# Optimization experiments

Hardware: AMD Instinct MI355X
Metric: run time of the kernel (lower is better)

Reference implementation:

```python
import jax, jax.numpy as jnp
import numpy as np

K = 5  # kernel_size per dim
# 2^dim = 4 active degree-1 B-spline products per edge (dim=2)
BITS = jnp.array([[0, 0], [1, 0], [0, 1], [1, 1]], dtype=jnp.int32)  # [S,2]


def spline_basis(edge_attr):
    """Open B-spline basis, degree=1, dim=2, kernel_size=5 per dim.
    Returns basis weights [E,S] and flattened kernel indices [E,S]."""
    v = edge_attr * (K - 1)                 # scale pseudo-coords to knot grid
    i0 = jnp.floor(v)
    f = v - i0                              # fractional part, [E,2]
    # per-dim linear weights: f for bit=1, (1-f) for bit=0
    w = jnp.where(BITS[None] == 1, f[:, None, :], 1.0 - f[:, None, :])  # [E,S,2]
    basis = w[..., 0] * w[..., 1]           # [E,S]
    idx = jnp.minimum(i0.astype(jnp.int32)[:, None, :] + BITS[None], K - 1)  # [E,S,2]
    kidx = idx[..., 0] + K * idx[..., 1]    # flatten 2D kernel index -> [0,25)
    return basis, kidx


def spline_conv(x, src, dst, basis, kidx, W, root, bias, n):
    # transform-then-gather: y[n,k,:] = x[n] @ W[k]
    y = jnp.einsum('ni,kio->nko', x, W)                 # [N,25,out]
    g = y[src[:, None], kidx]                           # gather [E,S,out]
    msg = jnp.einsum('es,eso->eo', basis, g)            # weighted sum over S
    agg = jax.ops.segment_sum(msg, dst, num_segments=n)  # scatter-add to targets
    return agg + x @ root + bias                        # root weight + bias


def setup_inputs() -> dict:
    key = jax.random.key(0)
    ks = jax.random.split(key, 8)
    N, E, IN, H, OUT = 50000, 400000, 32, 64, 64
    x = jax.random.normal(ks[0], (N, IN), jnp.float32)
    edge_index = jax.random.randint(ks[1], (2, E), 0, N, dtype=jnp.int32)
    edge_attr = jax.random.uniform(ks[2], (E, 2), jnp.float32)

    def glorot(k, shape):
        fan = shape[-2] + shape[-1]
        return jax.random.normal(k, shape, jnp.float32) * jnp.sqrt(2.0 / fan)

    W1 = glorot(ks[3], (K * K, IN, H));  root1 = glorot(ks[4], (IN, H));  b1 = jnp.zeros((H,), jnp.float32)
    W2 = glorot(ks[5], (K * K, H, OUT)); root2 = glorot(ks[6], (H, OUT)); b2 = jnp.zeros((OUT,), jnp.float32)
    fc_w = glorot(ks[7], (OUT, 3));      fc_b = jnp.zeros((3,), jnp.float32)
    return dict(x=x, edge_index=edge_index, edge_attr=edge_attr,
                W1=W1, root1=root1, b1=b1, W2=W2, root2=root2, b2=b2,
                fc_w=fc_w, fc_b=fc_b)


def reference(x, edge_index, edge_attr, W1, root1, b1, W2, root2, b2, fc_w, fc_b):
    # eval-mode forward (dropout is identity at inference)
    n = x.shape[0]
    src, dst = edge_index[0], edge_index[1]
    basis, kidx = spline_basis(edge_attr)
    h = jax.nn.relu(spline_conv(x, src, dst, basis, kidx, W1, root1, b1, n))
    h = jax.nn.relu(spline_conv(h, src, dst, basis, kidx, W2, root2, b2, n))
    return h @ fc_w + fc_b
```

## Files before the change

kernel.cpp:

```cpp
#include <hip/hip_runtime.h>
#include <stdint.h>

typedef __attribute__((ext_vector_type(8))) short short8;
typedef __attribute__((ext_vector_type(4))) float f32x4;
typedef __attribute__((ext_vector_type(4))) unsigned short ushort4v;

#define CHUNK 512

__device__ __forceinline__ unsigned short f2bf(float f) {
    unsigned int u = __float_as_uint(f);
    u = (u + 0x7FFFu + ((u >> 16) & 1u)) >> 16;
    return (unsigned short)u;
}
__device__ __forceinline__ float bf2f(unsigned short h) {
    return __uint_as_float(((unsigned int)h) << 16);
}
__device__ __forceinline__ int cell_of(float ax, float ay) {
    int c0 = (int)floorf(ax * 4.f); c0 = min(max(c0, 0), 3);
    int c1 = (int)floorf(ay * 4.f); c1 = min(max(c1, 0), 3);
    return c0 + 4 * c1;
}

__global__ __launch_bounds__(256) void zero_kernel(int* __restrict__ p, int n) {
    int t = blockIdx.x * 256 + threadIdx.x;
    if (t < n) p[t] = 0;
}

template<int KIN>
__device__ __forceinline__ void pack_cell_elem(const float* __restrict__ W,
                                               unsigned short* __restrict__ pkc, int u) {
    constexpr int KCH = KIN / 8;
    if (u >= 16 * 4 * KCH * 512) return;
    int low9 = u & 511;
    int grp  = u >> 9;
    int kc = grp % KCH; grp /= KCH;
    int c  = grp & 3;
    int cell = grp >> 2;
    int lane = low9 >> 3, j = low9 & 7;
    int k = kc * 32 + (lane >> 4) * 8 + j;
    int t = k / KIN, i = k % KIN;
    int k0 = (cell & 3) + (t & 1);   if (k0 > 4) k0 = 4;
    int k1 = (cell >> 2) + (t >> 1); if (k1 > 4) k1 = 4;
    float val = W[((size_t)(k0 + 5 * k1) * KIN + i) * 64 + (c * 16 + (lane & 15))];
    pkc[u] = f2bf(val);
}

template<int KIN>
__device__ __forceinline__ void pack_root_elem(const float* __restrict__ root,
                                               unsigned short* __restrict__ pkr, int u) {
    constexpr int KCHr = KIN / 32;
    if (u >= 4 * KCHr * 512) return;
    int low9 = u & 511;
    int grp  = u >> 9;
    int lane = low9 >> 3, j = low9 & 7;
    int kc = grp % KCHr, c = grp / KCHr;
    int k = kc * 32 + (lane >> 4) * 8 + j;
    int o = c * 16 + (lane & 15);
    float v = root[(size_t)k * 64 + o];
    unsigned short h = f2bf(v);
    pkr[(size_t)(grp * 2) * 512 + low9]     = h;
    pkr[(size_t)(grp * 2 + 1) * 512 + low9] = f2bf(v - bf2f(h));
}

__global__ __launch_bounds__(256) void prep_kernel(
    const float* __restrict__ attr, const int* __restrict__ dst,
    int* __restrict__ hist, int* __restrict__ dhist, int E,
    const float* __restrict__ W1, const float* __restrict__ W2,
    const float* __restrict__ root1, const float* __restrict__ root2,
    unsigned short* __restrict__ pkc1, unsigned short* __restrict__ pkc2,
    unsigned short* __restrict__ pkr1, unsigned short* __restrict__ pkr2,
    const float* __restrict__ x, unsigned short* __restrict__ xb, int n4,
    int EB)
{
    __shared__ int wcnt[4][16];
    int b = blockIdx.x;
    if (b < EB) {
        int e = b * 256 + threadIdx.x;
        int lane = threadIdx.x & 63, wave = threadIdx.x >> 6;
        int cell = -1;
        if (e < E) {
            float2 a = reinterpret_cast<const float2*>(attr)[e];
            cell = cell_of(a.x, a.y);
            atomicAdd(&dhist[dst[e]], 1);
        }
        #pragma unroll
        for (int c = 0; c < 16; c++) {
            unsigned long long m = __ballot(cell == c);
            if (lane == 0) wcnt[wave][c] = __popcll(m);
        }
        __syncthreads();
        if (threadIdx.x < 16) {
            int c = threadIdx.x;
            int tot = wcnt[0][c] + wcnt[1][c] + wcnt[2][c] + wcnt[3][c];
            if (tot) atomicAdd(&hist[c], tot);
        }
        return;
    }
    b -= EB;
    if (b < 512)  { pack_cell_elem<32>(W1, pkc1, b * 256 + threadIdx.x); return; }
    b -= 512;
    if (b < 1024) { pack_cell_elem<64>(W2, pkc2, b * 256 + threadIdx.x); return; }
    b -= 1024;
    if (b < 8)    { pack_root_elem<32>(root1, pkr1, b * 256 + threadIdx.x); return; }
    b -= 8;
    if (b < 16)   { pack_root_elem<64>(root2, pkr2, b * 256 + threadIdx.x); return; }
    b -= 16;
    {
        int t = b * 256 + threadIdx.x;
        if (t < n4) {
            float4 v = reinterpret_cast<const float4*>(x)[t];
            ushort4v o = { f2bf(v.x), f2bf(v.y), f2bf(v.z), f2bf(v.w) };
            reinterpret_cast<ushort4v*>(xb)[t] = o;
        }
    }
}

__global__ __launch_bounds__(1024) void scanAB_kernel(
    const int* __restrict__ dhist, int* __restrict__ nof, int* __restrict__ bsum,
    int Np1, int* __restrict__ done,
    const int* __restrict__ hist, int* __restrict__ off_e, int* __restrict__ off_b,
    int* __restrict__ cursor, int* __restrict__ bbase, int NB)
{
    __shared__ int wsum[16];
    int tid = threadIdx.x, lane = tid & 63, w = tid >> 6;
    int i = blockIdx.x * 1024 + tid;
    int v = (i < Np1) ? dhist[i] : 0;
    int s = v;
    #pragma unroll
    for (int off = 1; off < 64; off <<= 1) {
        int t = __shfl_up(s, off);
        if (lane >= off) s += t;
    }
    if (lane == 63) wsum[w] = s;
    __syncthreads();
    if (tid == 0) {
        int a = 0;
        #pragma unroll
        for (int k = 0; k < 16; k++) { int t = wsum[k]; wsum[k] = a; a += t; }
        bsum[blockIdx.x] = a;
    }
    __syncthreads();
    if (i < Np1) nof[i] = wsum[w] + s - v;

    __shared__ int amLast;
    __shared__ int lds_b[256];
    __shared__ int lds_h[16];
    __threadfence();
    if (tid == 0) amLast = (atomicAdd(done, 1) == gridDim.x - 1);
    __syncthreads();
    if (!amLast) return;
    __threadfence();
    if (tid < NB) lds_b[tid] = bsum[tid];
    if (tid < 16) lds_h[tid] = hist[tid];
    __syncthreads();
    if (tid == 0) {
        int a = 0;
        for (int k = 0; k < NB; k++) { int t = lds_b[k]; bbase[k] = a; a += t; }
        int se = 0, sb = 0;
        for (int c = 0; c < 16; c++) {
            off_e[c] = se; off_b[c] = sb; cursor[c] = se;
            se += lds_h[c]; sb += (lds_h[c] + CHUNK - 1) / CHUNK;
        }
        off_e[16] = se; off_b[16] = sb;
    }
}

__global__ __launch_bounds__(256) void scatter_kernel(const float* __restrict__ attr,
                                                      const int* __restrict__ src,
                                                      const int* __restrict__ dst,
                                                      const int* __restrict__ nof,
                                                      const int* __restrict__ bbase,
                                                      int4* __restrict__ emeta,
                                                      int* __restrict__ cursor,
                                                      int* __restrict__ dhist, int E) {
    __shared__ int wcnt[4][16];
    __shared__ int wbase[4][16];
    int e = blockIdx.x * 256 + threadIdx.x;
    int lane = threadIdx.x & 63, wave = threadIdx.x >> 6;
    int cell = -1;
    float2 a = {0.f, 0.f};
    int mp = 0, sv = 0;
    if (e < E) {
        a = reinterpret_cast<const float2*>(attr)[e];
        cell = cell_of(a.x, a.y);
        int d = dst[e];
        int rank = atomicSub(&dhist[d], 1) - 1;
        mp = nof[d] + bbase[d >> 10] + rank;
        sv = src[e];
    }
    int myrank = 0;
    #pragma unroll
    for (int c = 0; c < 16; c++) {
        unsigned long long m = __ballot(cell == c);
        if (cell == c) myrank = __popcll(m & ((1ull << lane) - 1ull));
        if (lane == 0) wcnt[wave][c] = __popcll(m);
    }
    __syncthreads();
    if (threadIdx.x < 16) {
        int c = threadIdx.x;
        int t0 = wcnt[0][c], t1 = wcnt[1][c], t2 = wcnt[2][c], t3 = wcnt[3][c];
        int tot = t0 + t1 + t2 + t3;
        int g = tot ? atomicAdd(&cursor[c], tot) : 0;
        wbase[0][c] = g;
        wbase[1][c] = g + t0;
        wbase[2][c] = g + t0 + t1;
        wbase[3][c] = g + t0 + t1 + t2;
    }
    __syncthreads();
    if (e < E) {
        int slot = wbase[wave][cell] + myrank;
        emeta[slot] = make_int4(sv, mp, __float_as_int(a.x), __float_as_int(a.y));
    }
}

template<int KIN>
__global__ __launch_bounds__(256) void layer_kernel(
    const unsigned short* __restrict__ Xb,
    const unsigned short* __restrict__ pkr, float* __restrict__ rt,
    const float* __restrict__ bias, int N, int RG,
    const unsigned short* __restrict__ pkc, unsigned short* __restrict__ msg,
    const int4* __restrict__ emeta,
    const int* __restrict__ off_e, const int* __restrict__ off_b)
{
    constexpr int KCHr = KIN / 32;
    constexpr int KCH  = 4 * KCHr;
    constexpr int NT   = CHUNK / 64;
    __shared__ unsigned short Blds[4 * KCH * 512];

    const int lane = threadIdx.x & 63;
    const int wave = threadIdx.x >> 6;
    const int lrow = lane & 15, lch = lane >> 4;

    if (blockIdx.x < RG) {
        const int mbase = blockIdx.x * 64 + wave * 16;
        short8 afrag[KCHr];
        {
            int row = mbase + lrow;
            if (row > N - 1) row = N - 1;
            const unsigned short* ap = Xb + (size_t)row * KIN + lch * 8;
            #pragma unroll
            for (int kc = 0; kc < KCHr; kc++)
                afrag[kc] = *reinterpret_cast<const short8*>(ap + kc * 32);
        }
        f32x4 acc[4];
        #pragma unroll
        for (int c = 0; c < 4; c++) acc[c] = (f32x4){0.f, 0.f, 0.f, 0.f};
        #pragma unroll
        for (int c = 0; c < 4; c++) {
            #pragma unroll
            for (int kc = 0; kc < KCHr; kc++) {
                short8 bh = *reinterpret_cast<const short8*>(pkr + ((size_t)(c * KCHr + kc) * 2    ) * 512 + lane * 8);
                short8 bl = *reinterpret_cast<const short8*>(pkr + ((size_t)(c * KCHr + kc) * 2 + 1) * 512 + lane * 8);
                acc[c] = __builtin_amdgcn_mfma_f32_16x16x32_bf16(afrag[kc], bh, acc[c], 0, 0, 0);
                acc[c] = __builtin_amdgcn_mfma_f32_16x16x32_bf16(afrag[kc], bl, acc[c], 0, 0, 0);
            }
        }
        #pragma unroll
        for (int c = 0; c < 4; c++) {
            int o = c * 16 + lrow;
            float bv = bias[o];
            #pragma unroll
            for (int r = 0; r < 4; r++) {
                int m = mbase + lch * 4 + r;
                if (m < N) rt[(size_t)m * 64 + o] = acc[c][r] + bv;
            }
        }
        return;
    }

    const int b = blockIdx.x - RG;
    if (b >= off_b[16]) return;
    int cell = 0;
    #pragma unroll
    for (int c = 1; c < 16; c++) cell += (b >= off_b[c]);
    const int chunk = b - off_b[cell];

    {
        const short8* sp = reinterpret_cast<const short8*>(pkc + (size_t)cell * (4 * KCH * 512));
        short8* dp = reinterpret_cast<short8*>(Blds);
        #pragma unroll
        for (int p = 0; p < KCH; p++)
            dp[p * 256 + threadIdx.x] = sp[p * 256 + threadIdx.x];
    }

    const int ebeg = off_e[cell];
    const int eend = off_e[cell + 1];
    const int base = ebeg + chunk * CHUNK;
    const float c0f = (float)(cell & 3), c1f = (float)(cell >> 2);

    int4 em[2];
    short8 xf[2][KCHr];

    {
        int sl0 = base + wave * 16 + lrow;
        em[0] = emeta[sl0 < eend ? sl0 : ebeg];
        const unsigned short* xp = Xb + (size_t)em[0].x * KIN + lch * 8;
        #pragma unroll
        for (int kcr = 0; kcr < KCHr; kcr++)
            xf[0][kcr] = *reinterpret_cast<const short8*>(xp + kcr * 32);
        int sl1 = base + (4 + wave) * 16 + lrow;
        em[1] = emeta[sl1 < eend ? sl1 : ebeg];
    }

    __syncthreads();

    #pragma unroll
    for (int tt = 0; tt < NT; tt++) {
        const int cur = tt & 1, nxt = cur ^ 1;
        const int tbase = base + (tt * 4 + wave) * 16;
        const bool anyv = tbase < eend;

        const int mp = (tbase + lrow < eend) ? em[cur].y : -1;
        float wv[4];
        {
            float f0 = __int_as_float(em[cur].z) * 4.f - c0f;
            float f1 = __int_as_float(em[cur].w) * 4.f - c1f;
            wv[0] = (1.f - f0) * (1.f - f1); wv[1] = f0 * (1.f - f1);
            wv[2] = (1.f - f0) * f1;         wv[3] = f0 * f1;
        }

        if (tt + 2 < NT) {
            int sl = base + ((tt + 2) * 4 + wave) * 16 + lrow;
            em[cur] = emeta[sl < eend ? sl : ebeg];
        }
        if (tt + 1 < NT) {
            const unsigned short* xp = Xb + (size_t)em[nxt].x * KIN + lch * 8;
            #pragma unroll
            for (int kcr = 0; kcr < KCHr; kcr++)
                xf[nxt][kcr] = *reinterpret_cast<const short8*>(xp + kcr * 32);
        }

        if (anyv) {
            float wr[4][4];
            int pv[4];
            #pragma unroll
            for (int r = 0; r < 4; r++) {
                int er = lch * 4 + r;
                #pragma unroll
                for (int t = 0; t < 4; t++) wr[t][r] = __shfl(wv[t], er);
                pv[r] = __shfl(mp, er);
            }

            #pragma unroll
            for (int c = 0; c < 4; c++) {
                f32x4 acc[4];
                #pragma unroll
                for (int t = 0; t < 4; t++) acc[t] = (f32x4){0.f, 0.f, 0.f, 0.f};
                #pragma unroll
                for (int t = 0; t < 4; t++) {
                    #pragma unroll
                    for (int kcr = 0; kcr < KCHr; kcr++) {
                        short8 bf = *reinterpret_cast<const short8*>(
                            &Blds[(size_t)((c * KCH) + (t * KCHr + kcr)) * 512 + lane * 8]);
                        acc[t] = __builtin_amdgcn_mfma_f32_16x16x32_bf16(xf[cur][kcr], bf, acc[t], 0, 0, 0);
                    }
                }
                const int o = c * 16 + lrow;
                #pragma unroll
                for (int r = 0; r < 4; r++) {
                    if (pv[r] >= 0) {
                        float m = wr[0][r] * acc[0][r] + wr[1][r] * acc[1][r]
                                + wr[2][r] * acc[2][r] + wr[3][r] * acc[3][r];
                        msg[(size_t)pv[r] * 64 + o] = f2bf(m);
                    }
                }
            }
        }
    }
}

template<int MODE>
__global__ __launch_bounds__(256) void segsum_kernel(
    const unsigned short* __restrict__ msg, const float* __restrict__ rt,
    const int* __restrict__ nof, const int* __restrict__ bbase,
    unsigned short* __restrict__ hout,
    const float* __restrict__ fcw, const float* __restrict__ fcb,
    float* __restrict__ out, int N)
{
    int n = blockIdx.x * 4 + (threadIdx.x >> 6);
    if (n >= N) return;
    int lane = threadIdx.x & 63;
    float acc = rt[(size_t)n * 64 + lane];
    int jb = nof[n]     + bbase[n >> 10];
    int je = nof[n + 1] + bbase[(n + 1) >> 10];
    int j = jb;
    for (; j + 3 < je; j += 4) {
        float a0 = bf2f(msg[(size_t)(j + 0) * 64 + lane]);
        float a1 = bf2f(msg[(size_t)(j + 1) * 64 + lane]);
        float a2 = bf2f(msg[(size_t)(j + 2) * 64 + lane]);
        float a3 = bf2f(msg[(size_t)(j + 3) * 64 + lane]);
        acc += a0; acc += a1; acc += a2; acc += a3;
    }
    for (; j < je; j++) acc += bf2f(msg[(size_t)j * 64 + lane]);
    acc = fmaxf(acc, 0.f);
    if (MODE == 0) {
        hout[(size_t)n * 64 + lane] = f2bf(acc);
    } else {
        float p0 = acc * fcw[lane * 3 + 0];
        float p1 = acc * fcw[lane * 3 + 1];
        float p2 = acc * fcw[lane * 3 + 2];
        #pragma unroll
        for (int off = 32; off; off >>= 1) {
            p0 += __shfl_xor(p0, off);
            p1 += __shfl_xor(p1, off);
            p2 += __shfl_xor(p2, off);
        }
        if (lane == 0) {
            out[(size_t)n * 3 + 0] = p0 + fcb[0];
            out[(size_t)n * 3 + 1] = p1 + fcb[1];
            out[(size_t)n * 3 + 2] = p2 + fcb[2];
        }
    }
}

extern "C" void kernel_launch(void* const* d_in, const int* in_sizes, int n_in,
                              void* d_out, int out_size, void* d_ws, size_t ws_size,
                              hipStream_t stream)
{
    const float* x     = (const float*)d_in[0];
    const int*   ei    = (const int*)  d_in[1];
    const float* attr  = (const float*)d_in[2];
    const float* W1    = (const float*)d_in[3];
    const float* root1 = (const float*)d_in[4];
    const float* b1    = (const float*)d_in[5];
    const float* W2    = (const float*)d_in[6];
    const float* root2 = (const float*)d_in[7];
    const float* b2    = (const float*)d_in[8];
    const float* fcw   = (const float*)d_in[9];
    const float* fcb   = (const float*)d_in[10];

    const int N = in_sizes[0] / 32;
    const int E = in_sizes[1] / 2;
    const int* srcp = ei;
    const int* dstp = ei + E;

    char* wsp = (char*)d_ws;
    auto alloc = [&](size_t bytes) -> char* {
        char* p = wsp;
        wsp += (bytes + 255) & ~(size_t)255;
        return p;
    };
    const int NB = (N + 1 + 1023) / 1024;

    float*          rt       = (float*)alloc((size_t)N * 64 * 4);
    unsigned short* xb       = (unsigned short*)alloc((size_t)N * 32 * 2);
    unsigned short* h1b      = (unsigned short*)alloc((size_t)N * 64 * 2);
    unsigned short* pkr1     = (unsigned short*)alloc((size_t)4 * 1 * 2 * 512 * 2);
    unsigned short* pkr2     = (unsigned short*)alloc((size_t)4 * 2 * 2 * 512 * 2);
    unsigned short* pkc1     = (unsigned short*)alloc((size_t)16 * 4 * 4 * 512 * 2);
    unsigned short* pkc2     = (unsigned short*)alloc((size_t)16 * 4 * 8 * 512 * 2);
    int4*           emeta    = (int4*)alloc((size_t)E * 16);
    int*            nof      = (int*)alloc((size_t)(N + 1) * 4);
    int*            bsum     = (int*)alloc((size_t)NB * 4);
    int*            bbase    = (int*)alloc((size_t)NB * 4);
    int*            off_e    = (int*)alloc(17 * 4);
    int*            off_b    = (int*)alloc(17 * 4);
    int*            cursor   = (int*)alloc(16 * 4);
    int*            zbase    = (int*)alloc((size_t)(16 + N + 1 + 1) * 4);
    int*            hist     = zbase;
    int*            dhist    = zbase + 16;
    int*            done     = zbase + 16 + N + 1;
    unsigned short* msg      = (unsigned short*)alloc((size_t)E * 64 * 2);

    const int ZN = 16 + N + 1 + 1;
    zero_kernel<<<(ZN + 255) / 256, 256, 0, stream>>>(zbase, ZN);

    const int EB = (E + 255) / 256;
    const int CB = (N * 8 + 255) / 256;
    const int prep_grid = EB + 512 + 1024 + 8 + 16 + CB;

    prep_kernel<<<prep_grid, 256, 0, stream>>>(attr, dstp, hist, dhist, E,
                                               W1, W2, root1, root2,
                                               pkc1, pkc2, pkr1, pkr2,
                                               x, xb, N * 8, EB);
    scanAB_kernel<<<NB, 1024, 0, stream>>>(dhist, nof, bsum, N + 1, done,
                                           hist, off_e, off_b, cursor, bbase, NB);
    scatter_kernel<<<EB, 256, 0, stream>>>(attr, srcp, dstp, nof, bbase, emeta, cursor, dhist, E);

    const int RG = (N + 63) / 64;
    const int lgrid = RG + (E + CHUNK - 1) / CHUNK + 16;
    const int sgrid = (N + 3) / 4;

    layer_kernel<32><<<lgrid, 256, 0, stream>>>(xb, pkr1, rt, b1, N, RG,
                                                pkc1, msg, emeta, off_e, off_b);
    segsum_kernel<0><<<sgrid, 256, 0, stream>>>(msg, rt, nof, bbase, h1b, fcw, fcb, (float*)d_out, N);

    layer_kernel<64><<<lgrid, 256, 0, stream>>>(h1b, pkr2, rt, b2, N, RG,
                                                pkc2, msg, emeta, off_e, off_b);
    segsum_kernel<1><<<sgrid, 256, 0, stream>>>(msg, rt, nof, bbase, nullptr, fcw, fcb, (float*)d_out, N);
}
```

Baseline: 197.3 us.

## Sort edges by kernel cell and source block for gather locality

```diff
diff --git a/kernel.cpp b/kernel.cpp
--- a/kernel.cpp
+++ b/kernel.cpp
@@ -6,6 +6,7 @@
 typedef __attribute__((ext_vector_type(4))) unsigned short ushort4v;
 
 #define CHUNK 512
+#define SBSH  9
 
 __device__ __forceinline__ unsigned short f2bf(float f) {
     unsigned int u = __float_as_uint(f);
@@ -63,8 +64,9 @@
 }
 
 __global__ __launch_bounds__(256) void prep_kernel(
-    const float* __restrict__ attr, const int* __restrict__ dst,
-    int* __restrict__ hist, int* __restrict__ dhist, int E,
+    const float* __restrict__ attr, const int* __restrict__ src,
+    const int* __restrict__ dst,
+    int* __restrict__ chist, int* __restrict__ dhist, int E, int NSB,
     const float* __restrict__ W1, const float* __restrict__ W2,
     const float* __restrict__ root1, const float* __restrict__ root2,
     unsigned short* __restrict__ pkc1, unsigned short* __restrict__ pkc2,
@@ -72,27 +74,14 @@
     const float* __restrict__ x, unsigned short* __restrict__ xb, int n4,
     int EB)
 {
-    __shared__ int wcnt[4][16];
     int b = blockIdx.x;
     if (b < EB) {
         int e = b * 256 + threadIdx.x;
-        int lane = threadIdx.x & 63, wave = threadIdx.x >> 6;
-        int cell = -1;
         if (e < E) {
             float2 a = reinterpret_cast<const float2*>(attr)[e];
-            cell = cell_of(a.x, a.y);
+            int cell = cell_of(a.x, a.y);
+            atomicAdd(&chist[cell * NSB + (src[e] >> SBSH)], 1);
             atomicAdd(&dhist[dst[e]], 1);
-        }
-        #pragma unroll
-        for (int c = 0; c < 16; c++) {
-            unsigned long long m = __ballot(cell == c);
-            if (lane == 0) wcnt[wave][c] = __popcll(m);
-        }
-        __syncthreads();
-        if (threadIdx.x < 16) {
-            int c = threadIdx.x;
-            int tot = wcnt[0][c] + wcnt[1][c] + wcnt[2][c] + wcnt[3][c];
-            if (tot) atomicAdd(&hist[c], tot);
         }
         return;
     }
@@ -118,8 +107,9 @@
 __global__ __launch_bounds__(1024) void scanAB_kernel(
     const int* __restrict__ dhist, int* __restrict__ nof, int* __restrict__ bsum,
     int Np1, int* __restrict__ done,
-    const int* __restrict__ hist, int* __restrict__ off_e, int* __restrict__ off_b,
-    int* __restrict__ cursor, int* __restrict__ bbase, int NB)
+    int* __restrict__ chist, int NSB,
+    int* __restrict__ off_e, int* __restrict__ off_b,
+    int* __restrict__ bbase, int NB)
 {
     __shared__ int wsum[16];
     int tid = threadIdx.x, lane = tid & 63, w = tid >> 6;
@@ -144,24 +134,43 @@
 
     __shared__ int amLast;
     __shared__ int lds_b[256];
-    __shared__ int lds_h[16];
+    __shared__ int ctot[16];
     __threadfence();
     if (tid == 0) amLast = (atomicAdd(done, 1) == gridDim.x - 1);
     __syncthreads();
     if (!amLast) return;
     __threadfence();
     if (tid < NB) lds_b[tid] = bsum[tid];
-    if (tid < 16) lds_h[tid] = hist[tid];
     __syncthreads();
     if (tid == 0) {
         int a = 0;
         for (int k = 0; k < NB; k++) { int t = lds_b[k]; bbase[k] = a; a += t; }
+    }
+    if (tid < 16) {
+        int a = 0;
+        for (int sblk = 0; sblk < NSB; sblk++) {
+            int idx = tid * NSB + sblk;
+            int t = chist[idx];
+            chist[idx] = a;
+            a += t;
+        }
+        ctot[tid] = a;
+    }
+    __syncthreads();
+    if (tid == 0) {
         int se = 0, sb = 0;
         for (int c = 0; c < 16; c++) {
-            off_e[c] = se; off_b[c] = sb; cursor[c] = se;
-            se += lds_h[c]; sb += (lds_h[c] + CHUNK - 1) / CHUNK;
+            off_e[c] = se; off_b[c] = sb;
+            se += ctot[c]; sb += (ctot[c] + CHUNK - 1) / CHUNK;
         }
         off_e[16] = se; off_b[16] = sb;
+    }
+    __syncthreads();
+    if (tid < 16) {
+        int basec = 0;
+        for (int c = 0; c < tid; c++) basec += ctot[c];
+        if (basec)
+            for (int sblk = 0; sblk < NSB; sblk++) chist[tid * NSB + sblk] += basec;
     }
 }
 
@@ -171,46 +180,18 @@
                                                       const int* __restrict__ nof,
                                                       const int* __restrict__ bbase,
                                                       int4* __restrict__ emeta,
-                                                      int* __restrict__ cursor,
+                                                      int* __restrict__ chist, int NSB,
                                                       int* __restrict__ dhist, int E) {
-    __shared__ int wcnt[4][16];
-    __shared__ int wbase[4][16];
     int e = blockIdx.x * 256 + threadIdx.x;
-    int lane = threadIdx.x & 63, wave = threadIdx.x >> 6;
-    int cell = -1;
-    float2 a = {0.f, 0.f};
-    int mp = 0, sv = 0;
-    if (e < E) {
-        a = reinterpret_cast<const float2*>(attr)[e];
-        cell = cell_of(a.x, a.y);
-        int d = dst[e];
-        int rank = atomicSub(&dhist[d], 1) - 1;
-        mp = nof[d] + bbase[d >> 10] + rank;
-        sv = src[e];
-    }
-    int myrank = 0;
-    #pragma unroll
-    for (int c = 0; c < 16; c++) {
-        unsigned long long m = __ballot(cell == c);
-        if (cell == c) myrank = __popcll(m & ((1ull << lane) - 1ull));
-        if (lane == 0) wcnt[wave][c] = __popcll(m);
-    }
-    __syncthreads();
-    if (threadIdx.x < 16) {
-        int c = threadIdx.x;
-        int t0 = wcnt[0][c], t1 = wcnt[1][c], t2 = wcnt[2][c], t3 = wcnt[3][c];
-        int tot = t0 + t1 + t2 + t3;
-        int g = tot ? atomicAdd(&cursor[c], tot) : 0;
-        wbase[0][c] = g;
-        wbase[1][c] = g + t0;
-        wbase[2][c] = g + t0 + t1;
-        wbase[3][c] = g + t0 + t1 + t2;
-    }
-    __syncthreads();
-    if (e < E) {
-        int slot = wbase[wave][cell] + myrank;
-        emeta[slot] = make_int4(sv, mp, __float_as_int(a.x), __float_as_int(a.y));
-    }
+    if (e >= E) return;
+    float2 a = reinterpret_cast<const float2*>(attr)[e];
+    int cell = cell_of(a.x, a.y);
+    int d = dst[e];
+    int rank = atomicSub(&dhist[d], 1) - 1;
+    int mp = nof[d] + bbase[d >> 10] + rank;
+    int sv = src[e];
+    int slot = atomicAdd(&chist[cell * NSB + (sv >> SBSH)], 1);
+    emeta[slot] = make_int4(sv, mp, __float_as_int(a.x), __float_as_int(a.y));
 }
 
 template<int KIN>
@@ -440,7 +421,8 @@
         wsp += (bytes + 255) & ~(size_t)255;
         return p;
     };
-    const int NB = (N + 1 + 1023) / 1024;
+    const int NB  = (N + 1 + 1023) / 1024;
+    const int NSB = (N + (1 << SBSH) - 1) >> SBSH;
 
     float*          rt       = (float*)alloc((size_t)N * 64 * 4);
     unsigned short* xb       = (unsigned short*)alloc((size_t)N * 32 * 2);
@@ -455,27 +437,27 @@
     int*            bbase    = (int*)alloc((size_t)NB * 4);
     int*            off_e    = (int*)alloc(17 * 4);
     int*            off_b    = (int*)alloc(17 * 4);
-    int*            cursor   = (int*)alloc(16 * 4);
-    int*            zbase    = (int*)alloc((size_t)(16 + N + 1 + 1) * 4);
-    int*            hist     = zbase;
-    int*            dhist    = zbase + 16;
-    int*            done     = zbase + 16 + N + 1;
+    int*            zbase    = (int*)alloc((size_t)(16 * NSB + N + 1 + 1) * 4);
+    int*            chist    = zbase;
+    int*            dhist    = zbase + 16 * NSB;
+    int*            done     = zbase + 16 * NSB + N + 1;
     unsigned short* msg      = (unsigned short*)alloc((size_t)E * 64 * 2);
 
-    const int ZN = 16 + N + 1 + 1;
+    const int ZN = 16 * NSB + N + 1 + 1;
     zero_kernel<<<(ZN + 255) / 256, 256, 0, stream>>>(zbase, ZN);
 
     const int EB = (E + 255) / 256;
     const int CB = (N * 8 + 255) / 256;
     const int prep_grid = EB + 512 + 1024 + 8 + 16 + CB;
 
-    prep_kernel<<<prep_grid, 256, 0, stream>>>(attr, dstp, hist, dhist, E,
+    prep_kernel<<<prep_grid, 256, 0, stream>>>(attr, srcp, dstp, chist, dhist, E, NSB,
                                                W1, W2, root1, root2,
                                                pkc1, pkc2, pkr1, pkr2,
                                                x, xb, N * 8, EB);
     scanAB_kernel<<<NB, 1024, 0, stream>>>(dhist, nof, bsum, N + 1, done,
-                                           hist, off_e, off_b, cursor, bbase, NB);
-    scatter_kernel<<<EB, 256, 0, stream>>>(attr, srcp, dstp, nof, bbase, emeta, cursor, dhist, E);
+                                           chist, NSB, off_e, off_b, bbase, NB);
+    scatter_kernel<<<EB, 256, 0, stream>>>(attr, srcp, dstp, nof, bbase, emeta,
+                                           chist, NSB, dhist, E);
 
     const int RG = (N + 63) / 64;
     const int lgrid = RG + (E + CHUNK - 1) / CHUNK + 16;
```

New measurement: 307.0 us. 55.6% more time.
